# Performance work log

Measured on AMD Instinct MI355X. Metric: run time of the kernel, lower is better.

The kernel has to match this reference:

```python
import jax, jax.numpy as jnp
import numpy as np

N_QUBITS = 10
N_LAYERS = 4
BATCH = 16384


def setup_inputs() -> dict:
    key = jax.random.key(0)
    k1, k2 = jax.random.split(key)
    x = jax.random.normal(k1, (BATCH, N_LAYERS * N_QUBITS), dtype=jnp.float32)
    weight = jax.random.normal(k2, (N_LAYERS, N_QUBITS, 2), dtype=jnp.float32) * 0.1
    return {"x": x, "weight": weight}


def _apply_1q(state, U, q):
    # state: [B, 2, 2, ..., 2] (axis 1+q is wire q); U: [B, 2, 2] batched unitary
    s = jnp.moveaxis(state, 1 + q, -1)
    s = jnp.einsum('bij,b...j->b...i', U, s)
    return jnp.moveaxis(s, -1, 1 + q)


def _apply_cnot(state, c, t):
    # CNOT with control wire c, target wire t: flip target where control==1
    s = jnp.moveaxis(state, (1 + c, 1 + t), (-2, -1))
    s = jnp.stack([s[..., 0, :], s[..., 1, ::-1]], axis=-2)
    return jnp.moveaxis(s, (-2, -1), (1 + c, 1 + t))


def _ry(theta):
    # theta: [...]; returns [..., 2, 2] real rotation matrix RY(theta)
    c, s = jnp.cos(theta * 0.5), jnp.sin(theta * 0.5)
    return jnp.stack([jnp.stack([c, -s], -1), jnp.stack([s, c], -1)], -2)


def _forward(x, weight):
    B = x.shape[0]
    # data re-uploading angles: atan(x) * pi, shape [B, L, Q]
    a = jnp.arctan(x.reshape(B, N_LAYERS, N_QUBITS)) * jnp.pi
    Rin = _ry(a).astype(jnp.complex64)                       # [B,L,Q,2,2]
    w0, w1 = weight[..., 0], weight[..., 1]                  # [L,Q]
    # RZ(w0) = diag(e^{-i w0/2}, e^{+i w0/2}); composing scales rows of RY
    phase = jnp.stack([jnp.exp(-0.5j * w0), jnp.exp(0.5j * w0)], -1)  # [L,Q,2]
    Rw = _ry(w1).astype(jnp.complex64)                       # [L,Q,2,2]
    M = Rin * phase[None, :, :, :, None]                     # RZ(w0) @ RY(a)
    U = jnp.einsum('lqij,blqjk->blqik', Rw, M)               # RY(w1)@RZ(w0)@RY(a)

    # |0...0> state, shape [B] + [2]*N_QUBITS
    state = jnp.zeros((B,) + (2,) * N_QUBITS, jnp.complex64)
    state = state.at[(slice(None),) + (0,) * N_QUBITS].set(1.0)

    for l in range(N_LAYERS):
        for q in range(N_QUBITS):
            state = _apply_1q(state, U[:, l, q], q)
        for q in range(N_QUBITS):
            state = _apply_cnot(state, q, (q + 1) % N_QUBITS)

    probs = state.real ** 2 + state.imag ** 2
    outs = []
    for q in range(N_QUBITS):
        p = jnp.moveaxis(probs, 1 + q, 1).reshape(B, 2, -1).sum(-1)
        outs.append(p[:, 0] - p[:, 1])  # <Z_q> = P(0) - P(1)
    return jnp.stack(outs, -1).astype(jnp.float32)


def reference(x, weight):
    return _forward(x, weight)
```

## Files before the change

### kernel.cpp

```cpp
#include <hip/hip_runtime.h>
#include <hip/hip_fp16.h>
#include <math.h>

#define NQ 10
#define NL 4
#define NA (NQ * NL)
#define PI_F 3.14159265358979323846f
#define INV_2PI_F 0.15915494309189535f

typedef _Float16 h2 __attribute__((ext_vector_type(2)));

template <int SR, int SI>
__device__ __forceinline__ unsigned cmul_sg(unsigned c, unsigned s) {
  unsigned d;
  if constexpr (SR > 0) {
    asm("v_pk_mul_f16 %0, %1, %2 op_sel_hi:[0,1]" : "=v"(d) : "v"(c), "v"(s));
  } else {
    asm("v_pk_mul_f16 %0, %1, %2 op_sel_hi:[0,1] neg_lo:[1,0] neg_hi:[1,0]"
        : "=v"(d) : "v"(c), "v"(s));
  }
  if constexpr (SI > 0) {
    asm("v_pk_fma_f16 %0, %1, %2, %0 op_sel:[1,1,0] op_sel_hi:[1,0,1] neg_lo:[1,0,0]"
        : "+v"(d) : "v"(c), "v"(s));
  } else {
    asm("v_pk_fma_f16 %0, %1, %2, %0 op_sel:[1,1,0] op_sel_hi:[1,0,1] neg_hi:[1,0,0]"
        : "+v"(d) : "v"(c), "v"(s));
  }
  return d;
}

template <int SR, int SI>
__device__ __forceinline__ unsigned cfma_sg(unsigned c, unsigned s, unsigned acc) {
  unsigned d;
  if constexpr (SR > 0) {
    asm("v_pk_fma_f16 %0, %1, %2, %3 op_sel_hi:[0,1,1]"
        : "=v"(d) : "v"(c), "v"(s), "v"(acc));
  } else {
    asm("v_pk_fma_f16 %0, %1, %2, %3 op_sel_hi:[0,1,1] neg_lo:[1,0,0] neg_hi:[1,0,0]"
        : "=v"(d) : "v"(c), "v"(s), "v"(acc));
  }
  if constexpr (SI > 0) {
    asm("v_pk_fma_f16 %0, %1, %2, %0 op_sel:[1,1,0] op_sel_hi:[1,0,1] neg_lo:[1,0,0]"
        : "+v"(d) : "v"(c), "v"(s));
  } else {
    asm("v_pk_fma_f16 %0, %1, %2, %0 op_sel:[1,1,0] op_sel_hi:[1,0,1] neg_hi:[1,0,0]"
        : "+v"(d) : "v"(c), "v"(s));
  }
  return d;
}

template <int MASK>
__device__ __forceinline__ int ishfl_xor(int v) {
  if constexpr (MASK == 1) {
    return __builtin_amdgcn_update_dpp(v, v, 0xB1, 0xF, 0xF, true);
  } else if constexpr (MASK == 2) {
    return __builtin_amdgcn_update_dpp(v, v, 0x4E, 0xF, 0xF, true);
  } else if constexpr (MASK == 4) {
    return __builtin_amdgcn_ds_swizzle(v, 0x101F);
  } else if constexpr (MASK == 8) {
    return __builtin_amdgcn_update_dpp(v, v, 0x128, 0xF, 0xF, true);
  } else if constexpr (MASK == 16) {
    return __builtin_amdgcn_ds_swizzle(v, 0x401F);
  } else {
    return __shfl_xor(v, MASK, 64);
  }
}

template <int MASK, int E>
__device__ __forceinline__ int ishfl_xor_e(int v) {
  if constexpr (E == 1) {
    if constexpr (MASK == 1) {
      return __builtin_amdgcn_ds_swizzle(v, 0x041F);
    } else if constexpr (MASK == 2) {
      return __builtin_amdgcn_ds_swizzle(v, 0x081F);
    } else if constexpr (MASK == 8) {
      return __builtin_amdgcn_ds_swizzle(v, 0x201F);
    } else {
      return ishfl_xor<MASK>(v);
    }
  } else {
    return ishfl_xor<MASK>(v);
  }
}

template <int MASK>
__device__ __forceinline__ float fshfl_xor(float v) {
  return __int_as_float(ishfl_xor<MASK>(__float_as_int(v)));
}

__device__ __forceinline__ unsigned readlane_u(unsigned v, int l) {
  return (unsigned)__builtin_amdgcn_readlane((int)v, l);
}

__device__ __forceinline__ float wave_sum_h(float v) {
  v += fshfl_xor<1>(v);
  v += fshfl_xor<2>(v);
  v += fshfl_xor<4>(v);
  v += fshfl_xor<8>(v);
  v += fshfl_xor<16>(v);
  v += fshfl_xor<32>(v);
  return v;
}

__device__ __forceinline__ unsigned pack_h2_rtn(float re, float im) {
  return (unsigned)__half_as_ushort(__float2half(re)) |
         ((unsigned)__half_as_ushort(__float2half(im)) << 16);
}

template <int LB>
__device__ __forceinline__ void cross_gate2(unsigned (&sv)[2][16],
                                            const unsigned (&u00)[2],
                                            const unsigned (&u01)[2], int lane) {
  const bool bit = (lane & (1 << LB)) != 0;
  unsigned A[2], B[2];
#pragma unroll
  for (int e = 0; e < 2; ++e) {
    A[e] = bit ? (u00[e] ^ 0x80000000u) : u00[e];
    B[e] = bit ? (u01[e] ^ 0x00008000u) : u01[e];
  }
#pragma unroll
  for (int r = 0; r < 16; ++r) {
    unsigned p0 = (unsigned)ishfl_xor_e<(1 << LB), 0>((int)sv[0][r]);
    unsigned p1 = (unsigned)ishfl_xor_e<(1 << LB), 1>((int)sv[1][r]);
    sv[0][r] = cfma_sg<1, 1>(B[0], p0, cmul_sg<1, 1>(A[0], sv[0][r]));
    sv[1][r] = cfma_sg<1, 1>(B[1], p1, cmul_sg<1, 1>(A[1], sv[1][r]));
  }
}

template <int LB>
__device__ __forceinline__ void cross_gate2_r0(unsigned (&sv)[2][16],
                                               const unsigned (&u00)[2],
                                               const unsigned (&u01)[2], int lane) {
  const bool bit = (lane & (1 << LB)) != 0;
  {
    const unsigned A = bit ? (u00[0] ^ 0x80000000u) : u00[0];
    const unsigned B = bit ? (u01[0] ^ 0x00008000u) : u01[0];
    unsigned p = (unsigned)ishfl_xor_e<(1 << LB), 0>((int)sv[0][0]);
    sv[0][0] = cfma_sg<1, 1>(B, p, cmul_sg<1, 1>(A, sv[0][0]));
  }
  {
    const unsigned A = bit ? (u00[1] ^ 0x80000000u) : u00[1];
    const unsigned B = bit ? (u01[1] ^ 0x00008000u) : u01[1];
    unsigned p = (unsigned)ishfl_xor_e<(1 << LB), 1>((int)sv[1][0]);
    sv[1][0] = cfma_sg<1, 1>(B, p, cmul_sg<1, 1>(A, sv[1][0]));
  }
}

template <int RB>
__device__ __forceinline__ void local_gate2(unsigned (&sv)[2][16],
                                            const unsigned (&u00)[2],
                                            const unsigned (&u01)[2]) {
#pragma unroll
  for (int rlo = 0; rlo < 16; ++rlo) {
    if (rlo & (1 << RB)) continue;
    const int rhi = rlo | (1 << RB);
#pragma unroll
    for (int e = 0; e < 2; ++e) {
      unsigned lo = sv[e][rlo], hi = sv[e][rhi];
      sv[e][rlo] = cfma_sg<1, 1>(u01[e], hi, cmul_sg<1, 1>(u00[e], lo));
      sv[e][rhi] = cfma_sg<1, -1>(u00[e], hi, cmul_sg<-1, 1>(u01[e], lo));
    }
  }
}

template <int RB>
__device__ __forceinline__ void local_gate2_fill(unsigned (&sv)[2][16],
                                                 const unsigned (&u00)[2],
                                                 const unsigned (&u01)[2]) {
#pragma unroll
  for (int rlo = 0; rlo < 16; ++rlo) {
    if (rlo & ((2 << RB) - 1)) continue;
    const int rhi = rlo | (1 << RB);
#pragma unroll
    for (int e = 0; e < 2; ++e) {
      unsigned lo = sv[e][rlo];
      sv[e][rhi] = cmul_sg<-1, 1>(u01[e], lo);
      sv[e][rlo] = cmul_sg<1, 1>(u00[e], lo);
    }
  }
}

__device__ __forceinline__ void ring_step(unsigned (&sv)[2][16], int lane,
                                          int permSrc) {
#pragma unroll
  for (int r = 0; r < 16; ++r) {
    sv[0][r] = (unsigned)__shfl((int)sv[0][r], permSrc);
    sv[1][r] = (unsigned)__shfl((int)sv[1][r], permSrc);
  }
  {
    const bool c5 = (lane & 1) != 0;
#pragma unroll
    for (int r = 0; r < 8; ++r) {
#pragma unroll
      for (int e = 0; e < 2; ++e) {
        unsigned a = sv[e][r], b = sv[e][r + 8];
        sv[e][r] = c5 ? b : a;
        sv[e][r + 8] = c5 ? a : b;
      }
    }
  }
#pragma unroll
  for (int e = 0; e < 2; ++e) {
    unsigned t;
    t = sv[e][2]; sv[e][2] = sv[e][3]; sv[e][3] = t;
    t = sv[e][4]; sv[e][4] = sv[e][6]; sv[e][6] = sv[e][5]; sv[e][5] = sv[e][7]; sv[e][7] = t;
    t = sv[e][8]; sv[e][8] = sv[e][12]; sv[e][12] = sv[e][10]; sv[e][10] = sv[e][15]; sv[e][15] = t;
    t = sv[e][9]; sv[e][9] = sv[e][13]; sv[e][13] = sv[e][11]; sv[e][11] = sv[e][14]; sv[e][14] = t;
  }
#pragma unroll
  for (int r = 1; r < 16; r += 2) {
    sv[0][r] = (unsigned)ishfl_xor<32>((int)sv[0][r]);
    sv[1][r] = (unsigned)ishfl_xor<32>((int)sv[1][r]);
  }
}

__global__ __launch_bounds__(256, 4) void qsim_kernel(
    const float* __restrict__ x, const float* __restrict__ w,
    float* __restrict__ out, int batch) {
  const int lane = threadIdx.x & 63;
  const int wv = blockIdx.x * 4 + (threadIdx.x >> 6);
  const int permSrc = lane ^ (lane >> 1);

  float Pr = 0.f, Pi = 0.f, Qr = 0.f, Qi = 0.f;
  if (lane < NA) {
    float w0 = w[2 * lane], w1 = w[2 * lane + 1];
    float r0 = w0 * (0.5f * INV_2PI_F), r1 = w1 * (0.5f * INV_2PI_F);
    float sphi = __builtin_amdgcn_sinf(r0), cphi = __builtin_amdgcn_cosf(r0);
    float sw = __builtin_amdgcn_sinf(r1), cw = __builtin_amdgcn_cosf(r1);
    Pr = cw * cphi; Pi = -cw * sphi;
    Qr = sw * cphi; Qi = sw * sphi;
  }

  unsigned U00[2] = {0u, 0u}, U01[2] = {0u, 0u};
#pragma unroll
  for (int e = 0; e < 2; ++e) {
    const int wid = wv * 2 + e;
    const int widc = wid < batch ? wid : batch - 1;
    if (lane < NA) {
      float xv = x[widc * NA + lane];
      float rev = 0.25f * atanf(xv);
      float sa = __builtin_amdgcn_sinf(rev);
      float ca = __builtin_amdgcn_cosf(rev);
      float u00r = ca * Pr - sa * Qr;
      float u00i = ca * Pi - sa * Qi;
      float u01r = -(sa * Pr + ca * Qr);
      float u01i = -(sa * Pi + ca * Qi);
      U00[e] = pack_h2_rtn(u00r, u00i);
      U01[e] = pack_h2_rtn(u01r, u01i);
    }
  }

  unsigned sv[2][16];
#pragma unroll
  for (int r = 0; r < 16; ++r) { sv[0][r] = 0u; sv[1][r] = 0u; }
  if (lane == 0) { sv[0][0] = 0x3C00u; sv[1][0] = 0x3C00u; }

#define GET_U(j)                                                     \
  const unsigned u00[2] = {readlane_u(U00[0], (j)), readlane_u(U00[1], (j))}; \
  const unsigned u01[2] = {readlane_u(U01[0], (j)), readlane_u(U01[1], (j))}

  { GET_U(0); cross_gate2_r0<5>(sv, u00, u01, lane); }
  { GET_U(1); cross_gate2_r0<4>(sv, u00, u01, lane); }
  { GET_U(2); cross_gate2_r0<3>(sv, u00, u01, lane); }
  { GET_U(3); cross_gate2_r0<2>(sv, u00, u01, lane); }
  { GET_U(4); cross_gate2_r0<1>(sv, u00, u01, lane); }
  { GET_U(5); cross_gate2_r0<0>(sv, u00, u01, lane); }
  { GET_U(6); local_gate2_fill<3>(sv, u00, u01); }
  { GET_U(7); local_gate2_fill<2>(sv, u00, u01); }
  { GET_U(8); local_gate2_fill<1>(sv, u00, u01); }
  { GET_U(9); local_gate2_fill<0>(sv, u00, u01); }
  ring_step(sv, lane, permSrc);

#pragma unroll 1
  for (int l = 1; l < NL; ++l) {
    const int j0 = l * NQ;
    { GET_U(j0 + 0); cross_gate2<5>(sv, u00, u01, lane); }
    { GET_U(j0 + 1); cross_gate2<4>(sv, u00, u01, lane); }
    { GET_U(j0 + 2); cross_gate2<3>(sv, u00, u01, lane); }
    { GET_U(j0 + 3); cross_gate2<2>(sv, u00, u01, lane); }
    { GET_U(j0 + 4); cross_gate2<1>(sv, u00, u01, lane); }
    { GET_U(j0 + 5); cross_gate2<0>(sv, u00, u01, lane); }
    { GET_U(j0 + 6); local_gate2<3>(sv, u00, u01); }
    { GET_U(j0 + 7); local_gate2<2>(sv, u00, u01); }
    { GET_U(j0 + 8); local_gate2<1>(sv, u00, u01); }
    { GET_U(j0 + 9); local_gate2<0>(sv, u00, u01); }
    ring_step(sv, lane, permSrc);
  }
#undef GET_U

#pragma unroll
  for (int e = 0; e < 2; ++e) {
    const int wid = wv * 2 + e;
    float tot = 0.f, t0 = 0.f, t1 = 0.f, t2 = 0.f, t3 = 0.f;
#pragma unroll
    for (int r = 0; r < 16; ++r) {
      h2 a = __builtin_bit_cast(h2, sv[e][r]);
      tot = __builtin_amdgcn_fdot2(a, a, tot, false);
      if (r & 1) t0 = __builtin_amdgcn_fdot2(a, a, t0, false);
      if (r & 2) t1 = __builtin_amdgcn_fdot2(a, a, t1, false);
      if (r & 4) t2 = __builtin_amdgcn_fdot2(a, a, t2, false);
      if (r & 8) t3 = __builtin_amdgcn_fdot2(a, a, t3, false);
    }
    const float S3 = wave_sum_h(t3);
    const float S2 = wave_sum_h(t2);
    const float S1 = wave_sum_h(t1);
    const float S0 = wave_sum_h(t0);
    const float N = wave_sum_h(tot);
    const float invN = 1.0f / N;
    float v = tot, h;
    h = fshfl_xor<1>(v);  v = (lane & 1)  ? h - v : v + h;
    h = fshfl_xor<2>(v);  v = (lane & 2)  ? h - v : v + h;
    h = fshfl_xor<4>(v);  v = (lane & 4)  ? h - v : v + h;
    h = fshfl_xor<8>(v);  v = (lane & 8)  ? h - v : v + h;
    h = fshfl_xor<16>(v); v = (lane & 16) ? h - v : v + h;
    h = fshfl_xor<32>(v); v = (lane & 32) ? h - v : v + h;

    if (wid < batch) {
      float* o = out + wid * NQ;
      if (lane == 32) o[0] = v * invN;
      if (lane == 16) o[1] = v * invN;
      if (lane == 8)  o[2] = v * invN;
      if (lane == 4)  o[3] = v * invN;
      if (lane == 2)  o[4] = v * invN;
      if (lane == 1)  o[5] = v * invN;
      if (lane == 0) {
        o[6] = (v - 2.f * S3) * invN;
        o[7] = (v - 2.f * S2) * invN;
        o[8] = (v - 2.f * S1) * invN;
        o[9] = (v - 2.f * S0) * invN;
      }
    }
  }
}

extern "C" void kernel_launch(void* const* d_in, const int* in_sizes, int n_in,
                              void* d_out, int out_size, void* d_ws, size_t ws_size,
                              hipStream_t stream) {
  const float* x = (const float*)d_in[0];
  const float* w = (const float*)d_in[1];
  float* out = (float*)d_out;
  const int batch = in_sizes[0] / NA;
  const int waves = (batch + 1) / 2;
  const int blocks = (waves + 3) / 4;
  qsim_kernel<<<blocks, 256, 0, stream>>>(x, w, out, batch);
}
```

Before: 132.5 us.

## Defer ring-step lane-32 swap into next cross gate and batch shuffles

Drops the xor-32 shuffle on odd registers at the end of each ring step except the last. The following lane-bit-5 cross gate absorbs that permutation by swapping the roles of own and partner amplitudes for odd registers. Shuffles in the cross gates are now all issued before the arithmetic, and the ring-step register permutation is folded into one table-driven select. This removes 32 cross-lane ops per layer and lets shuffle latency overlap, at the cost of more live registers for the temporaries.

```diff
diff --git a/kernel.cpp b/kernel.cpp
--- a/kernel.cpp
+++ b/kernel.cpp
@@ -107,7 +107,7 @@
          ((unsigned)__half_as_ushort(__float2half(im)) << 16);
 }
 
-template <int LB>
+template <int LB, bool DEF = false>
 __device__ __forceinline__ void cross_gate2(unsigned (&sv)[2][16],
                                             const unsigned (&u00)[2],
                                             const unsigned (&u01)[2], int lane) {
@@ -118,12 +118,21 @@
     A[e] = bit ? (u00[e] ^ 0x80000000u) : u00[e];
     B[e] = bit ? (u01[e] ^ 0x00008000u) : u01[e];
   }
+  unsigned p[2][16];
 #pragma unroll
   for (int r = 0; r < 16; ++r) {
-    unsigned p0 = (unsigned)ishfl_xor_e<(1 << LB), 0>((int)sv[0][r]);
-    unsigned p1 = (unsigned)ishfl_xor_e<(1 << LB), 1>((int)sv[1][r]);
-    sv[0][r] = cfma_sg<1, 1>(B[0], p0, cmul_sg<1, 1>(A[0], sv[0][r]));
-    sv[1][r] = cfma_sg<1, 1>(B[1], p1, cmul_sg<1, 1>(A[1], sv[1][r]));
+    p[0][r] = (unsigned)ishfl_xor_e<(1 << LB), 0>((int)sv[0][r]);
+    p[1][r] = (unsigned)ishfl_xor_e<(1 << LB), 1>((int)sv[1][r]);
+  }
+#pragma unroll
+  for (int r = 0; r < 16; ++r) {
+    if (DEF && (r & 1)) {
+      sv[0][r] = cfma_sg<1, 1>(B[0], sv[0][r], cmul_sg<1, 1>(A[0], p[0][r]));
+      sv[1][r] = cfma_sg<1, 1>(B[1], sv[1][r], cmul_sg<1, 1>(A[1], p[1][r]));
+    } else {
+      sv[0][r] = cfma_sg<1, 1>(B[0], p[0][r], cmul_sg<1, 1>(A[0], sv[0][r]));
+      sv[1][r] = cfma_sg<1, 1>(B[1], p[1][r], cmul_sg<1, 1>(A[1], sv[1][r]));
+    }
   }
 }
 
@@ -132,17 +141,17 @@
                                                const unsigned (&u00)[2],
                                                const unsigned (&u01)[2], int lane) {
   const bool bit = (lane & (1 << LB)) != 0;
+  unsigned p0 = (unsigned)ishfl_xor_e<(1 << LB), 0>((int)sv[0][0]);
+  unsigned p1 = (unsigned)ishfl_xor_e<(1 << LB), 1>((int)sv[1][0]);
   {
     const unsigned A = bit ? (u00[0] ^ 0x80000000u) : u00[0];
     const unsigned B = bit ? (u01[0] ^ 0x00008000u) : u01[0];
-    unsigned p = (unsigned)ishfl_xor_e<(1 << LB), 0>((int)sv[0][0]);
-    sv[0][0] = cfma_sg<1, 1>(B, p, cmul_sg<1, 1>(A, sv[0][0]));
+    sv[0][0] = cfma_sg<1, 1>(B, p0, cmul_sg<1, 1>(A, sv[0][0]));
   }
   {
     const unsigned A = bit ? (u00[1] ^ 0x80000000u) : u00[1];
     const unsigned B = bit ? (u01[1] ^ 0x00008000u) : u01[1];
-    unsigned p = (unsigned)ishfl_xor_e<(1 << LB), 1>((int)sv[1][0]);
-    sv[1][0] = cfma_sg<1, 1>(B, p, cmul_sg<1, 1>(A, sv[1][0]));
+    sv[1][0] = cfma_sg<1, 1>(B, p1, cmul_sg<1, 1>(A, sv[1][0]));
   }
 }
 
@@ -181,36 +190,27 @@
 }
 
 __device__ __forceinline__ void ring_step(unsigned (&sv)[2][16], int lane,
-                                          int permSrc) {
+                                          int permSrc, bool apply_q9) {
+  unsigned t[2][16];
 #pragma unroll
   for (int r = 0; r < 16; ++r) {
-    sv[0][r] = (unsigned)__shfl((int)sv[0][r], permSrc);
-    sv[1][r] = (unsigned)__shfl((int)sv[1][r], permSrc);
-  }
-  {
-    const bool c5 = (lane & 1) != 0;
-#pragma unroll
-    for (int r = 0; r < 8; ++r) {
-#pragma unroll
-      for (int e = 0; e < 2; ++e) {
-        unsigned a = sv[e][r], b = sv[e][r + 8];
-        sv[e][r] = c5 ? b : a;
-        sv[e][r + 8] = c5 ? a : b;
-      }
-    }
-  }
-#pragma unroll
-  for (int e = 0; e < 2; ++e) {
-    unsigned t;
-    t = sv[e][2]; sv[e][2] = sv[e][3]; sv[e][3] = t;
-    t = sv[e][4]; sv[e][4] = sv[e][6]; sv[e][6] = sv[e][5]; sv[e][5] = sv[e][7]; sv[e][7] = t;
-    t = sv[e][8]; sv[e][8] = sv[e][12]; sv[e][12] = sv[e][10]; sv[e][10] = sv[e][15]; sv[e][15] = t;
-    t = sv[e][9]; sv[e][9] = sv[e][13]; sv[e][13] = sv[e][11]; sv[e][11] = sv[e][14]; sv[e][14] = t;
-  }
-#pragma unroll
-  for (int r = 1; r < 16; r += 2) {
-    sv[0][r] = (unsigned)ishfl_xor<32>((int)sv[0][r]);
-    sv[1][r] = (unsigned)ishfl_xor<32>((int)sv[1][r]);
+    t[0][r] = (unsigned)__shfl((int)sv[0][r], permSrc);
+    t[1][r] = (unsigned)__shfl((int)sv[1][r], permSrc);
+  }
+  const bool c5 = (lane & 1) != 0;
+  constexpr int m[16] = {0, 1, 3, 2, 6, 7, 5, 4, 12, 13, 15, 14, 10, 11, 9, 8};
+#pragma unroll
+  for (int j = 0; j < 16; ++j) {
+#pragma unroll
+    for (int e = 0; e < 2; ++e)
+      sv[e][j] = c5 ? t[e][m[j] ^ 8] : t[e][m[j]];
+  }
+  if (apply_q9) {
+#pragma unroll
+    for (int r = 1; r < 16; r += 2) {
+      sv[0][r] = (unsigned)ishfl_xor<32>((int)sv[0][r]);
+      sv[1][r] = (unsigned)ishfl_xor<32>((int)sv[1][r]);
+    }
   }
 }
 
@@ -269,12 +269,12 @@
   { GET_U(7); local_gate2_fill<2>(sv, u00, u01); }
   { GET_U(8); local_gate2_fill<1>(sv, u00, u01); }
   { GET_U(9); local_gate2_fill<0>(sv, u00, u01); }
-  ring_step(sv, lane, permSrc);
+  ring_step(sv, lane, permSrc, false);
 
 #pragma unroll 1
   for (int l = 1; l < NL; ++l) {
     const int j0 = l * NQ;
-    { GET_U(j0 + 0); cross_gate2<5>(sv, u00, u01, lane); }
+    { GET_U(j0 + 0); cross_gate2<5, true>(sv, u00, u01, lane); }
     { GET_U(j0 + 1); cross_gate2<4>(sv, u00, u01, lane); }
     { GET_U(j0 + 2); cross_gate2<3>(sv, u00, u01, lane); }
     { GET_U(j0 + 3); cross_gate2<2>(sv, u00, u01, lane); }
@@ -284,7 +284,7 @@
     { GET_U(j0 + 7); local_gate2<2>(sv, u00, u01); }
     { GET_U(j0 + 8); local_gate2<1>(sv, u00, u01); }
     { GET_U(j0 + 9); local_gate2<0>(sv, u00, u01); }
-    ring_step(sv, lane, permSrc);
+    ring_step(sv, lane, permSrc, (l == NL - 1));
   }
 #undef GET_U
 
```

After: 131.4 us (median of 2 runs). Within noise of the previous version (-0.8%).
